# Performance work log

Hardware: AMD Instinct MI355X
Metric: run time of the kernel (lower is better)

## Reference

```python
import jax, jax.numpy as jnp
import numpy as np

D_MODEL = 2048
D_STATE = 64
D_CONV = 4
EXPAND = 2
HEADDIM = 64
NGROUPS = 1
CHUNK = 64
D_INNER = D_MODEL * EXPAND          # 4096
NHEADS = D_INNER // HEADDIM         # 64
D_IN_PROJ = 2 * D_INNER + 2 * NGROUPS * D_STATE + NHEADS
BATCH, SEQLEN = 2, 4096
RMS_EPS = 1e-6


def elu_plus_one(x):
    return jax.nn.elu(x) + 1.0


def softplus(x):
    return jnp.where(x > 20, x, jnp.log1p(jnp.exp(x)))


def causal_conv1d(x, w, b):
    # x: (B, L, D), w: (K, D) depthwise kernel, b: (D,)
    Bsz, L, Dn = x.shape
    k = w.shape[0]
    xp = jnp.transpose(jnp.pad(x, ((0, 0), (k - 1, 0), (0, 0))), (0, 2, 1))  # (B, D, L+K-1)
    kern = jnp.transpose(w, (1, 0))[:, None, :]  # (D, 1, K)
    y = jax.lax.conv_general_dilated(xp, kern, (1,), 'VALID',
                                     feature_group_count=Dn,
                                     dimension_numbers=('NCH', 'OIH', 'NCH'))
    return jnp.transpose(y, (0, 2, 1)) + b


def ssd_chunked(q, k, v, a, chunk_size):
    # SSD / chunked linear attention with per-step scalar decay.
    # Recurrence: h_t = a_t * h_{t-1} + k_t v_t^T ; y_t = q_t @ h_t
    # q,k: (B,H,L,N); v: (B,H,L,P); a: (B,H,L) in (0,1)
    Bsz, H, L, N = q.shape
    S = chunk_size
    C = L // S
    qc = q.reshape(Bsz, H, C, S, N)
    kc = k.reshape(Bsz, H, C, S, N)
    vc = v.reshape(Bsz, H, C, S, -1)
    la = jnp.log(a).reshape(Bsz, H, C, S)
    cs = jnp.cumsum(la, axis=-1)                 # inclusive cumsum of log-decay within chunk
    causal = jnp.tril(jnp.ones((S, S), bool))
    # decay from position j to i (j<=i): exp(cs_i - cs_j)
    logdec = jnp.where(causal, cs[..., :, None] - cs[..., None, :], -jnp.inf)
    att = jnp.einsum('bhcsn,bhctn->bhcst', qc, kc) * jnp.exp(logdec)
    y_intra = jnp.einsum('bhcst,bhctp->bhcsp', att, vc)
    total = cs[..., -1]                           # (B,H,C) total log-decay per chunk
    k_scaled = kc * jnp.exp(total[..., None, None] - cs[..., None])
    states = jnp.einsum('bhcsn,bhcsp->bhcnp', k_scaled, vc)  # per-chunk state update
    d_t = jnp.moveaxis(jnp.exp(total), 2, 0)      # (C,B,H)
    s_t = jnp.moveaxis(states, 2, 0)              # (C,B,H,N,P)

    def step(h, inp):
        d, s = inp
        return d[..., None, None] * h + s, h      # emit state at chunk start

    _, h_prev = jax.lax.scan(step, jnp.zeros_like(s_t[0]), (d_t, s_t))
    h_prev = jnp.moveaxis(h_prev, 0, 2)           # (B,H,C,N,P)
    y_inter = jnp.einsum('bhcsn,bhcnp->bhcsp', qc * jnp.exp(cs)[..., None], h_prev)
    return (y_intra + y_inter).reshape(Bsz, H, L, -1)


def setup_inputs() -> dict:
    key = jax.random.key(0)
    k0, k1, k2, k3 = jax.random.split(key, 4)
    u = jax.random.normal(k0, (BATCH, SEQLEN, D_MODEL), jnp.float32)
    in_proj_w = jax.random.normal(k1, (D_MODEL, D_IN_PROJ), jnp.float32) / np.sqrt(D_MODEL)
    conv_weight = jax.random.normal(k2, (D_CONV, D_INNER), jnp.float32) / np.sqrt(D_CONV)
    conv_bias = jnp.zeros((D_INNER,), jnp.float32)
    A_log = jnp.log(jnp.linspace(1.0, 16.0, NHEADS)).astype(jnp.float32)
    dt_init = jnp.exp(jnp.linspace(np.log(0.001), np.log(0.1), NHEADS))
    dt_bias = (dt_init + jnp.log(-jnp.expm1(-dt_init))).astype(jnp.float32)
    D_param = jnp.ones((NHEADS,), jnp.float32)
    norm_scale = jnp.ones((D_INNER,), jnp.float32)
    out_proj_w = jax.random.normal(k3, (D_INNER, D_MODEL), jnp.float32) / np.sqrt(D_INNER)
    return dict(u=u, in_proj_w=in_proj_w, conv_weight=conv_weight, conv_bias=conv_bias,
                A_log=A_log, dt_bias=dt_bias, D_param=D_param, norm_scale=norm_scale,
                out_proj_w=out_proj_w)


def reference(u, in_proj_w, conv_weight, conv_bias, A_log, dt_bias, D_param, norm_scale, out_proj_w):
    Bsz, L, _ = u.shape
    zxBCdt = u @ in_proj_w
    splits = [D_INNER, 2 * D_INNER, 2 * D_INNER + NGROUPS * D_STATE, 2 * D_INNER + 2 * NGROUPS * D_STATE]
    z, x, B_proj, C_proj, dt_logits = jnp.split(zxBCdt, splits, axis=-1)
    x = jax.nn.silu(causal_conv1d(x, conv_weight, conv_bias))
    B_mat = elu_plus_one(B_proj.reshape(Bsz, L, NGROUPS, D_STATE))
    C_mat = elu_plus_one(C_proj.reshape(Bsz, L, NGROUPS, D_STATE))
    hpg = NHEADS // NGROUPS
    B_mat = jnp.repeat(B_mat, hpg, axis=2)   # (B,L,H,N)
    C_mat = jnp.repeat(C_mat, hpg, axis=2)
    dt = softplus(dt_logits + dt_bias)        # (B,L,H)
    a = jnp.exp(-dt * jnp.exp(A_log))         # (B,L,H), per-step decay
    x_heads = x.reshape(Bsz, L, NHEADS, HEADDIM)
    q = jnp.transpose(C_mat, (0, 2, 1, 3))
    k = jnp.transpose(B_mat, (0, 2, 1, 3))
    v = jnp.transpose(x_heads, (0, 2, 1, 3))
    a_t = jnp.transpose(a, (0, 2, 1))
    y = ssd_chunked(q, k, v, a_t, CHUNK)
    y = y + D_param[None, :, None, None] * v  # skip connection
    y = jnp.transpose(y, (0, 2, 1, 3)).reshape(Bsz, L, D_INNER)
    y = y * jax.lax.rsqrt(jnp.mean(y * y, axis=-1, keepdims=True) + RMS_EPS) * norm_scale
    y = y * jax.nn.silu(z)
    return y @ out_proj_w
```

## Files before the change

### kernel.cpp

```cpp
#include <hip/hip_runtime.h>
#include <hip/hip_bf16.h>
#include <cstdint>
#include <cstddef>

#define BATCH   2
#define SEQLEN  4096
#define DMODEL  2048
#define DINNER  4096
#define NHEADS  64
#define HEADDIM 64
#define DSTATE  64
#define CHUNK   64
#define NCHUNK  (SEQLEN/CHUNK)
#define DPROJ   8384
#define DPROJ_PAD 8448
#define MTOK    (BATCH*SEQLEN)
#define RMS_EPS 1e-6f

typedef __hip_bfloat16 bf16;
typedef __attribute__((ext_vector_type(8))) short bf16x8;
typedef __attribute__((ext_vector_type(4))) float f32x4;

__device__ __forceinline__ float siluf(float x) { return x / (1.f + expf(-x)); }
__device__ __forceinline__ float to_f(float x) { return x; }
__device__ __forceinline__ float to_f(bf16 x) { return __bfloat162float(x); }
__device__ __forceinline__ float bf2f(short s) { bf16 h; *(short*)&h = s; return __bfloat162float(h); }
__device__ __forceinline__ void from_f(float& d, float x) { d = x; }
__device__ __forceinline__ void from_f(bf16& d, float x) { d = __float2bfloat16(x); }

__device__ __forceinline__ void gload16(const void* g, void* l) {
  __builtin_amdgcn_global_load_lds(
      (const __attribute__((address_space(1))) void*)g,
      (__attribute__((address_space(3))) void*)l, 16, 0, 0);
}

template <typename TC, int KT>
__global__ __launch_bounds__(1024, 4) void gemm_w16(
    const bf16* __restrict__ A, int lda,
    const bf16* __restrict__ BT, int ldb,
    TC* __restrict__ C, int ldc, int gx) {
  __shared__ __align__(16) bf16 As[4 * 8192];
  __shared__ __align__(16) bf16 Bs[4 * 8192];
  const int tid  = threadIdx.x;
  const int lane = tid & 63;
  const int w    = tid >> 6;
  const int wm   = w >> 2;
  const int wn   = w & 3;
  const int lr   = lane & 15, lg = lane >> 4;
  const int fo   = 8 * (lg ^ ((lr >> 1) & 3));

  int nwg = gridDim.x;
  int bid = (int)blockIdx.x;
  int idx = (bid & 7) * (nwg >> 3) + (bid >> 3);
  int spos = idx % (8 * gx);
  const int m0 = ((idx / (8 * gx)) * 8 + (spos & 7)) * 256;
  const int n0 = (spos >> 3) * 256;

  const int srow = tid >> 2;
  const int ce   = 8 * ((tid & 3) ^ ((tid >> 3) & 3));
  const bf16* pA = A  + (size_t)(m0 + srow) * lda + ce;
  const bf16* pB = BT + (size_t)(n0 + srow) * ldb + ce;
  const int wofs = w * 512;
  const int aRd = (wm * 64 + lr) * 32 + fo;
  const int bRd = (wn * 64 + lr) * 32 + fo;

#define STAGE_A(kt) gload16(pA + ((kt) << 5), As + (((kt) & 3) << 13) + wofs)
#define STAGE_B(kt) gload16(pB + ((kt) << 5), Bs + (((kt) & 3) << 13) + wofs)

  f32x4 acc[4][4];
#pragma unroll
  for (int m = 0; m < 4; ++m)
#pragma unroll
    for (int n = 0; n < 4; ++n) acc[m][n] = (f32x4){0.f, 0.f, 0.f, 0.f};

  bf16x8 fr[2][8];

#define RDFRAG(P, SL) do {                                                    \
    const bf16* Ab_ = As + ((SL) << 13);                                      \
    const bf16* Bb_ = Bs + ((SL) << 13);                                      \
    _Pragma("unroll")                                                         \
    for (int n = 0; n < 4; ++n) fr[P][4 + n] = *(const bf16x8*)&Bb_[bRd + n * 512]; \
    _Pragma("unroll")                                                         \
    for (int m = 0; m < 4; ++m) fr[P][m] = *(const bf16x8*)&Ab_[aRd + m * 512]; \
  } while (0)

#define KB(T, P, DOSTAGE, DOPF, VMC) do {                                     \
    if (DOSTAGE) { STAGE_A((T) + 3); STAGE_B((T) + 3); }                      \
    asm volatile("s_waitcnt lgkmcnt(0)" ::: "memory");                        \
    __builtin_amdgcn_sched_barrier(0);                                        \
    __builtin_amdgcn_s_setprio(1);                                            \
    _Pragma("unroll")                                                         \
    for (int m = 0; m < 4; ++m)                                               \
      _Pragma("unroll")                                                       \
      for (int n = 0; n < 4; ++n)                                             \
        acc[m][n] = __builtin_amdgcn_mfma_f32_16x16x32_bf16(fr[P][m], fr[P][4 + n], acc[m][n], 0, 0, 0); \
    __builtin_amdgcn_s_setprio(0);                                            \
    if (DOPF) {                                                               \
      asm volatile("s_waitcnt vmcnt(" #VMC ")" ::: "memory");                 \
      __builtin_amdgcn_sched_barrier(0);                                      \
      RDFRAG(1 - (P), ((T) + 1) & 3);                                         \
    }                                                                         \
    __builtin_amdgcn_s_barrier();                                             \
    __builtin_amdgcn_sched_barrier(0);                                        \
  } while (0)

  STAGE_A(0); STAGE_B(0); STAGE_A(1); STAGE_B(1); STAGE_A(2); STAGE_B(2);
  asm volatile("s_waitcnt vmcnt(4)" ::: "memory");
  __builtin_amdgcn_s_barrier();
  __builtin_amdgcn_sched_barrier(0);
  RDFRAG(0, 0);

  for (int t4 = 0; t4 < KT - 4; t4 += 4) {
    KB(t4 + 0, 0, true, true, 4);
    KB(t4 + 1, 1, true, true, 4);
    KB(t4 + 2, 0, true, true, 4);
    KB(t4 + 3, 1, true, true, 4);
  }
  KB(KT - 4, 0, true,  true,  4);
  KB(KT - 3, 1, false, true,  2);
  KB(KT - 2, 0, false, true,  0);
  KB(KT - 1, 1, false, false, 0);
#undef KB
#undef RDFRAG
#undef STAGE_A
#undef STAGE_B

  if constexpr (__is_same(TC, bf16)) {
    bf16* Ws = (w < 8 ? As : Bs) + (w & 7) * 4096;
#pragma unroll
    for (int m = 0; m < 4; ++m)
#pragma unroll
      for (int n = 0; n < 4; ++n)
#pragma unroll
        for (int reg = 0; reg < 4; ++reg) {
          int row = m * 16 + lg * 4 + reg;
          int slot = (n * 2 + (lr >> 3)) ^ (row & 7);
          Ws[row * 64 + slot * 8 + (lr & 7)] = __float2bfloat16(acc[m][n][reg]);
        }
    asm volatile("s_waitcnt lgkmcnt(0)" ::: "memory");
#pragma unroll
    for (int i = 0; i < 8; ++i) {
      int row = i * 8 + (lane >> 3);
      bf16x8 v = *(const bf16x8*)&Ws[row * 64 + ((lane & 7) ^ (lane >> 3)) * 8];
      int gcol = n0 + wn * 64 + (lane & 7) * 8;
      *(bf16x8*)&((bf16*)C)[(size_t)(m0 + wm * 64 + row) * ldc + gcol] = v;
    }
  } else {
#pragma unroll
    for (int m = 0; m < 4; ++m)
#pragma unroll
      for (int n = 0; n < 4; ++n) {
        int col = n0 + wn * 64 + n * 16 + lr;
        size_t rbase = (size_t)(m0 + wm * 64 + m * 16 + lg * 4);
#pragma unroll
        for (int reg = 0; reg < 4; ++reg)
          from_f(C[(rbase + reg) * ldc + col], acc[m][n][reg]);
      }
  }
}

template <typename TC, bool MASK>
__global__ __launch_bounds__(256) void gemm_mfma(
    const bf16* __restrict__ A, int lda,
    const bf16* __restrict__ BT, int ldb,
    TC* __restrict__ C, int ldc, int Kdim, int Nvalid) {
  __shared__ __align__(16) bf16 As[128 * 32];
  __shared__ __align__(16) bf16 Bs[128 * 32];
  const int tid  = threadIdx.x;
  const int lane = tid & 63;
  const int w    = tid >> 6;
  const int m0 = blockIdx.y * 128;
  const int n0 = blockIdx.x * 128;

  const int rs0 = w * 32 + (lane >> 2);
  const int ce  = 8 * ((lane & 3) ^ ((lane >> 2) & 3));
  const int fo  = 8 * ((lane >> 4) ^ (lane & 3));
  const int lr  = lane & 15, lg = lane >> 4;
  const int wr = w >> 1, wc = w & 1;

  f32x4 acc[4][4];
#pragma unroll
  for (int m = 0; m < 4; ++m)
#pragma unroll
    for (int n = 0; n < 4; ++n) acc[m][n] = (f32x4){0.f, 0.f, 0.f, 0.f};

  const size_t arow0 = (size_t)(m0 + rs0) * lda;
  const size_t arow1 = (size_t)(m0 + rs0 + 16) * lda;
  const size_t brow0 = (size_t)(n0 + rs0) * ldb;
  const size_t brow1 = (size_t)(n0 + rs0 + 16) * ldb;
  bf16* lA0 = &As[(w * 2 + 0) * 512];
  bf16* lA1 = &As[(w * 2 + 1) * 512];
  bf16* lB0 = &Bs[(w * 2 + 0) * 512];
  bf16* lB1 = &Bs[(w * 2 + 1) * 512];

  for (int k0 = 0; k0 < Kdim; k0 += 32) {
    __syncthreads();
    gload16(A + arow0 + k0 + ce, lA0);
    gload16(A + arow1 + k0 + ce, lA1);
    gload16(BT + brow0 + k0 + ce, lB0);
    gload16(BT + brow1 + k0 + ce, lB1);
    __syncthreads();
    bf16x8 af[4], bfr[4];
#pragma unroll
    for (int m = 0; m < 4; ++m)
      af[m] = *(const bf16x8*)&As[(wr * 64 + m * 16 + lr) * 32 + fo];
#pragma unroll
    for (int n = 0; n < 4; ++n)
      bfr[n] = *(const bf16x8*)&Bs[(wc * 64 + n * 16 + lr) * 32 + fo];
#pragma unroll
    for (int m = 0; m < 4; ++m)
#pragma unroll
      for (int n = 0; n < 4; ++n)
        acc[m][n] = __builtin_amdgcn_mfma_f32_16x16x32_bf16(af[m], bfr[n], acc[m][n], 0, 0, 0);
  }

#pragma unroll
  for (int m = 0; m < 4; ++m)
#pragma unroll
    for (int n = 0; n < 4; ++n) {
      int col = n0 + wc * 64 + n * 16 + lr;
      if (MASK && col >= Nvalid) continue;
      size_t rbase = (size_t)(m0 + wr * 64 + m * 16 + lg * 4);
#pragma unroll
      for (int reg = 0; reg < 4; ++reg)
        from_f(C[(rbase + reg) * ldc + col], acc[m][n][reg]);
    }
}

__global__ __launch_bounds__(256) void cast_bf16_kernel(
    const float* __restrict__ x, bf16* __restrict__ y) {
  size_t i = ((size_t)blockIdx.x * 256 + threadIdx.x) * 4;
  float4 v = *(const float4*)(x + i);
  y[i + 0] = __float2bfloat16(v.x);
  y[i + 1] = __float2bfloat16(v.y);
  y[i + 2] = __float2bfloat16(v.z);
  y[i + 3] = __float2bfloat16(v.w);
}

__global__ __launch_bounds__(256) void transpose_cast_kernel(
    const float* __restrict__ W, bf16* __restrict__ WT, int N, int K) {
  __shared__ float t[32][33];
  int n0 = blockIdx.x * 32, k0 = blockIdx.y * 32;
  int tx = threadIdx.x & 31, ty = threadIdx.x >> 5;
#pragma unroll
  for (int i = 0; i < 4; ++i) {
    int n = n0 + tx;
    t[ty + i * 8][tx] = (n < N) ? W[(size_t)(k0 + ty + i * 8) * N + n] : 0.f;
  }
  __syncthreads();
#pragma unroll
  for (int i = 0; i < 4; ++i) {
    int nn = ty + i * 8;
    WT[(size_t)(n0 + nn) * K + k0 + tx] = __float2bfloat16(t[tx][nn]);
  }
}

__global__ __launch_bounds__(256) void conv_silu_kernel(
    const bf16* __restrict__ zx, const float* __restrict__ cw,
    const float* __restrict__ cb, bf16* __restrict__ xc) {
  int idx = blockIdx.x * 256 + threadIdx.x;
  int d8 = (idx & 511) * 8;
  int g = idx >> 9;
  int m0 = g * 4;
  int l0 = m0 & (SEQLEN - 1);
  int b = m0 >> 12;
  bf16x8 rows[7];
  bf16x8 zvec;
#pragma unroll
  for (int j = 0; j < 8; ++j) zvec[j] = 0;
#pragma unroll
  for (int r = 0; r < 7; ++r) {
    int li = l0 - 3 + r;
    rows[r] = (li >= 0)
        ? *(const bf16x8*)&zx[(size_t)(b * SEQLEN + li) * DPROJ + DINNER + d8]
        : zvec;
  }
  float cwv[4][8], cbv[8];
#pragma unroll
  for (int k = 0; k < 4; ++k) {
    float4 a = *(const float4*)(cw + k * DINNER + d8);
    float4 bb = *(const float4*)(cw + k * DINNER + d8 + 4);
    cwv[k][0] = a.x; cwv[k][1] = a.y; cwv[k][2] = a.z; cwv[k][3] = a.w;
    cwv[k][4] = bb.x; cwv[k][5] = bb.y; cwv[k][6] = bb.z; cwv[k][7] = bb.w;
  }
  {
    float4 a = *(const float4*)(cb + d8);
    float4 bb = *(const float4*)(cb + d8 + 4);
    cbv[0] = a.x; cbv[1] = a.y; cbv[2] = a.z; cbv[3] = a.w;
    cbv[4] = bb.x; cbv[5] = bb.y; cbv[6] = bb.z; cbv[7] = bb.w;
  }
#pragma unroll
  for (int j = 0; j < 4; ++j) {
    float acc[8];
#pragma unroll
    for (int e = 0; e < 8; ++e) acc[e] = cbv[e];
#pragma unroll
    for (int k = 0; k < 4; ++k)
#pragma unroll
      for (int e = 0; e < 8; ++e) acc[e] += bf2f(rows[j + k][e]) * cwv[k][e];
    bf16x8 o;
#pragma unroll
    for (int e = 0; e < 8; ++e) { bf16 h = __float2bfloat16(siluf(acc[e])); o[e] = *(short*)&h; }
    *(bf16x8*)&xc[(size_t)(m0 + j) * DINNER + d8] = o;
  }
}

__global__ __launch_bounds__(256) void prep_cumsum_kernel(
    const bf16* __restrict__ zx, const float* __restrict__ A_log,
    const float* __restrict__ dt_bias, bf16* __restrict__ Bmb,
    bf16* __restrict__ Cmb, float* __restrict__ cs) {
  int bid = blockIdx.x;
  int c = bid & 63, b = bid >> 6;
  int m0 = b * SEQLEN + c * CHUNK;
  int tid = threadIdx.x;
  int s = tid >> 2, grp = (tid & 3) * 16;
  __shared__ float laT[64 * 65];
  __shared__ float segs[4][64];
  const bf16* row = zx + (size_t)(m0 + s) * DPROJ + 2 * DINNER;
  {
    union { bf16x8 v[2]; bf16 hh[16]; } u, o;
    u.v[0] = *(const bf16x8*)&row[grp];
    u.v[1] = *(const bf16x8*)&row[grp + 8];
#pragma unroll
    for (int i = 0; i < 16; ++i) {
      float bv = to_f(u.hh[i]);
      from_f(o.hh[i], bv > 0.f ? bv + 1.f : expf(bv));
    }
    *(bf16x8*)&Bmb[(size_t)(m0 + s) * 64 + grp] = o.v[0];
    *(bf16x8*)&Bmb[(size_t)(m0 + s) * 64 + grp + 8] = o.v[1];
    u.v[0] = *(const bf16x8*)&row[64 + grp];
    u.v[1] = *(const bf16x8*)&row[64 + grp + 8];
#pragma unroll
    for (int i = 0; i < 16; ++i) {
      float cv = to_f(u.hh[i]);
      from_f(o.hh[i], cv > 0.f ? cv + 1.f : expf(cv));
    }
    *(bf16x8*)&Cmb[(size_t)(m0 + s) * 64 + grp] = o.v[0];
    *(bf16x8*)&Cmb[(size_t)(m0 + s) * 64 + grp + 8] = o.v[1];
    u.v[0] = *(const bf16x8*)&row[128 + grp];
    u.v[1] = *(const bf16x8*)&row[128 + grp + 8];
#pragma unroll
    for (int i = 0; i < 16; ++i) {
      int j = grp + i;
      float dtl = to_f(u.hh[i]) + dt_bias[j];
      float dt = dtl > 20.f ? dtl : log1pf(expf(dtl));
      laT[j * 65 + s] = -dt * expf(A_log[j]);
    }
  }
  __syncthreads();
  int j = tid & 63, sg = tid >> 6;
  float p = 0.f;
#pragma unroll
  for (int i = 0; i < 16; ++i) p += laT[j * 65 + sg * 16 + i];
  segs[sg][j] = p;
  __syncthreads();
  float off = (sg > 0 ? segs[0][j] : 0.f) + (sg > 1 ? segs[1][j] : 0.f) +
              (sg > 2 ? segs[2][j] : 0.f);
  float acc = off;
#pragma unroll
  for (int i = 0; i < 16; ++i) {
    acc += laT[j * 65 + sg * 16 + i];
    cs[(size_t)(m0 + sg * 16 + i) * 64 + j] = acc;
  }
}

__global__ __launch_bounds__(256) void states_mfma(
    const bf16* __restrict__ Bmb, const bf16* __restrict__ xc,
    const float* __restrict__ cs, bf16* __restrict__ st) {
  int bid = blockIdx.x;
  int c = bid & 63, h = (bid >> 6) & 63, b = bid >> 12;
  int m0 = b * SEQLEN + c * CHUNK;
  int tid = threadIdx.x, lane = tid & 63, w = tid >> 6;
  int lr = lane & 15, lg = lane >> 4;
  __shared__ bf16 vT[64 * 72];
  __shared__ bf16 kT[64 * 72];
  int s4 = tid >> 2, c16 = (tid & 3) * 16;
  float cstot = cs[(size_t)(m0 + 63) * 64 + h];
  float ws = expf(cstot - cs[(size_t)(m0 + s4) * 64 + h]);
  {
    union { bf16x8 v[2]; bf16 hh[16]; } u;
    const bf16x8* pv = (const bf16x8*)&xc[(size_t)(m0 + s4) * DINNER + h * 64 + c16];
    u.v[0] = pv[0]; u.v[1] = pv[1];
#pragma unroll
    for (int i = 0; i < 16; ++i) vT[(c16 + i) * 72 + s4] = u.hh[i];
    const bf16x8* pk = (const bf16x8*)&Bmb[(size_t)(m0 + s4) * 64 + c16];
    u.v[0] = pk[0]; u.v[1] = pk[1];
#pragma unroll
    for (int i = 0; i < 16; ++i) kT[(c16 + i) * 72 + s4] = __float2bfloat16(to_f(u.hh[i]) * ws);
  }
  __syncthreads();
  f32x4 acc[4];
#pragma unroll
  for (int ct = 0; ct < 4; ++ct) acc[ct] = (f32x4){0.f, 0.f, 0.f, 0.f};
#pragma unroll
  for (int ks = 0; ks < 2; ++ks) {
    bf16x8 af = *(const bf16x8*)&vT[(w * 16 + lr) * 72 + ks * 32 + lg * 8];
#pragma unroll
    for (int ct = 0; ct < 4; ++ct) {
      bf16x8 bf_ = *(const bf16x8*)&kT[(ct * 16 + lr) * 72 + ks * 32 + lg * 8];
      acc[ct] = __builtin_amdgcn_mfma_f32_16x16x32_bf16(af, bf_, acc[ct], 0, 0, 0);
    }
  }
  size_t ob = (((size_t)(b * NHEADS + h)) * NCHUNK + c) * 4096;
#pragma unroll
  for (int ct = 0; ct < 4; ++ct) {
    int n = ct * 16 + lr;
#pragma unroll
    for (int r = 0; r < 4; ++r) {
      int p = w * 16 + lg * 4 + r;
      from_f(st[ob + (size_t)p * 64 + n], acc[ct][r]);
    }
  }
}

__global__ __launch_bounds__(256) void scan_kernel(
    const float* __restrict__ cs, bf16* __restrict__ st) {
  int bid = blockIdx.x;
  int bh = bid >> 2, qq = bid & 3;
  int b = bh >> 6, h = bh & 63;
  int tid = threadIdx.x;
  __shared__ float dec[64];
  if (tid < 64)
    dec[tid] = expf(cs[(size_t)(b * SEQLEN + tid * CHUNK + 63) * 64 + h]);
  int e0 = qq * 1024 + tid * 4;
  float hr[4] = {0.f, 0.f, 0.f, 0.f};
  size_t base = (size_t)bh * NCHUNK * 4096;
  typedef __attribute__((ext_vector_type(4))) short bf16x4;
  union U { bf16x4 v; bf16 hh[4]; };
  U buf[4];
  buf[0].v = *(bf16x4*)(st + base + 0 * 4096 + e0);
  buf[1].v = *(bf16x4*)(st + base + 1 * 4096 + e0);
  buf[2].v = *(bf16x4*)(st + base + 2 * 4096 + e0);
  __syncthreads();
#pragma unroll 4
  for (int c = 0; c < NCHUNK; ++c) {
    if (c + 3 < NCHUNK)
      buf[(c + 3) & 3].v = *(bf16x4*)(st + base + (size_t)(c + 3) * 4096 + e0);
    float d = dec[c];
    U out;
#pragma unroll
    for (int i = 0; i < 4; ++i) {
      float sv = to_f(buf[c & 3].hh[i]);
      from_f(out.hh[i], hr[i]);
      hr[i] = d * hr[i] + sv;
    }
    *(bf16x4*)(st + base + (size_t)c * 4096 + e0) = out.v;
  }
}

__global__ __launch_bounds__(256) void chunk_out_mfma(
    const bf16* __restrict__ Bmb, const bf16* __restrict__ Cmb,
    const bf16* __restrict__ xc, const float* __restrict__ cs,
    const bf16* __restrict__ st, const float* __restrict__ Dp,
    bf16* __restrict__ zx) {
  int bid = blockIdx.x;
  int c = bid & 63, h = (bid >> 6) & 63, b = bid >> 12;
  int m0 = b * SEQLEN + c * CHUNK;
  int tid = threadIdx.x, lane = tid & 63, w = tid >> 6;
  int lr = lane & 15, lg = lane >> 4;
  __shared__ bf16 qL[64 * 72];
  __shared__ bf16 kL[64 * 72];
  __shared__ bf16 A2[64 * 136];
  __shared__ bf16 B2[64 * 136];
  __shared__ float csl[64];
  int s4 = tid >> 2, c16 = (tid & 3) * 16;

  if (tid < 64) csl[tid] = cs[(size_t)(m0 + tid) * 64 + h];
  {
    const bf16x8* pq = (const bf16x8*)&Cmb[(size_t)(m0 + s4) * 64 + c16];
    *(bf16x8*)&qL[s4 * 72 + c16] = pq[0];
    *(bf16x8*)&qL[s4 * 72 + c16 + 8] = pq[1];
    const bf16x8* pk = (const bf16x8*)&Bmb[(size_t)(m0 + s4) * 64 + c16];
    *(bf16x8*)&kL[s4 * 72 + c16] = pk[0];
    *(bf16x8*)&kL[s4 * 72 + c16 + 8] = pk[1];
  }
  {
    union { bf16x8 v[2]; bf16 hh[16]; } u;
    const bf16x8* pv = (const bf16x8*)&xc[(size_t)(m0 + s4) * DINNER + h * 64 + c16];
    u.v[0] = pv[0]; u.v[1] = pv[1];
#pragma unroll
    for (int i = 0; i < 16; ++i) B2[(c16 + i) * 136 + s4] = u.hh[i];
  }
  {
    size_t hb = (((size_t)(b * NHEADS + h)) * NCHUNK + c) * 4096;
    const bf16x8* ph = (const bf16x8*)&st[hb + (size_t)s4 * 64 + c16];
    *(bf16x8*)&B2[s4 * 136 + 64 + c16] = ph[0];
    *(bf16x8*)&B2[s4 * 136 + 64 + c16 + 8] = ph[1];
  }
  __syncthreads();

  f32x4 acc1[4];
#pragma unroll
  for (int ct = 0; ct < 4; ++ct) acc1[ct] = (f32x4){0.f, 0.f, 0.f, 0.f};
#pragma unroll
  for (int ks = 0; ks < 2; ++ks) {
    bf16x8 af = *(const bf16x8*)&qL[(w * 16 + lr) * 72 + ks * 32 + lg * 8];
#pragma unroll
    for (int ct = 0; ct < 4; ++ct) {
      bf16x8 bf_ = *(const bf16x8*)&kL[(ct * 16 + lr) * 72 + ks * 32 + lg * 8];
      acc1[ct] = __builtin_amdgcn_mfma_f32_16x16x32_bf16(af, bf_, acc1[ct], 0, 0, 0);
    }
  }
  {
    float es = expf(csl[s4]);
    union { bf16x8 v[2]; bf16 hh[16]; } u;
    const bf16x8* pq = (const bf16x8*)&qL[s4 * 72 + c16];
    u.v[0] = pq[0]; u.v[1] = pq[1];
#pragma unroll
    for (int i = 0; i < 16; ++i) u.hh[i] = __float2bfloat16(to_f(u.hh[i]) * es);
    *(bf16x8*)&A2[s4 * 136 + 64 + c16] = u.v[0];
    *(bf16x8*)&A2[s4 * 136 + 64 + c16 + 8] = u.v[1];
  }
#pragma unroll
  for (int ct = 0; ct < 4; ++ct) {
    int t = ct * 16 + lr;
#pragma unroll
    for (int r = 0; r < 4; ++r) {
      int s = w * 16 + lg * 4 + r;
      float val = (t <= s) ? acc1[ct][r] * expf(csl[s] - csl[t]) : 0.f;
      A2[s * 136 + t] = __float2bfloat16(val);
    }
  }
  __syncthreads();

  float Dh = Dp[h];
  f32x4 acc2[4];
#pragma unroll
  for (int ct = 0; ct < 4; ++ct) {
    int p = ct * 16 + lr;
#pragma unroll
    for (int r = 0; r < 4; ++r)
      acc2[ct][r] = Dh * to_f(B2[p * 136 + (w * 16 + lg * 4 + r)]);
  }
#pragma unroll
  for (int ks = 0; ks < 4; ++ks) {
    bf16x8 af = *(const bf16x8*)&A2[(w * 16 + lr) * 136 + ks * 32 + lg * 8];
#pragma unroll
    for (int ct = 0; ct < 4; ++ct) {
      bf16x8 bf_ = *(const bf16x8*)&B2[(ct * 16 + lr) * 136 + ks * 32 + lg * 8];
      acc2[ct] = __builtin_amdgcn_mfma_f32_16x16x32_bf16(af, bf_, acc2[ct], 0, 0, 0);
    }
  }
  __syncthreads();
#pragma unroll
  for (int ct = 0; ct < 4; ++ct) {
    int p = ct * 16 + lr;
#pragma unroll
    for (int r = 0; r < 4; ++r)
      qL[(w * 16 + lg * 4 + r) * 72 + p] = __float2bfloat16(acc2[ct][r]);
  }
  __syncthreads();
  {
    const bf16x8* py = (const bf16x8*)&qL[s4 * 72 + c16];
    bf16x8* pg = (bf16x8*)&zx[(size_t)(m0 + s4) * DPROJ + DINNER + h * 64 + c16];
    pg[0] = py[0]; pg[1] = py[1];
  }
}

__global__ __launch_bounds__(256) void rmsnorm_gate_kernel(
    bf16* __restrict__ zx, const float* __restrict__ scale) {
  int m = blockIdx.x;
  int tid = threadIdx.x;
  bf16* row = zx + (size_t)m * DPROJ;
  float vals[16];
  float ss = 0.f;
#pragma unroll
  for (int g = 0; g < 2; ++g) {
    int d8 = (tid + g * 256) * 8;
    bf16x8 yv = *(const bf16x8*)&row[DINNER + d8];
#pragma unroll
    for (int j = 0; j < 8; ++j) {
      float y = bf2f(yv[j]);
      vals[g * 8 + j] = y;
      ss += y * y;
    }
  }
#pragma unroll
  for (int off = 32; off > 0; off >>= 1) ss += __shfl_down(ss, off, 64);
  __shared__ float red[4];
  if ((tid & 63) == 0) red[tid >> 6] = ss;
  __syncthreads();
  float tot = red[0] + red[1] + red[2] + red[3];
  float inv = rsqrtf(tot / (float)DINNER + RMS_EPS);
#pragma unroll
  for (int g = 0; g < 2; ++g) {
    int d8 = (tid + g * 256) * 8;
    bf16x8 zv = *(const bf16x8*)&row[d8];
    const float* sc = scale + d8;
    bf16x8 o;
#pragma unroll
    for (int j = 0; j < 8; ++j) {
      bf16 hh = __float2bfloat16(vals[g * 8 + j] * inv * sc[j] * siluf(bf2f(zv[j])));
      o[j] = *(short*)&hh;
    }
    *(bf16x8*)&row[DINNER + d8] = o;
  }
}

extern "C" void kernel_launch(void* const* d_in, const int* in_sizes, int n_in,
                              void* d_out, int out_size, void* d_ws, size_t ws_size,
                              hipStream_t stream) {
  const float* u       = (const float*)d_in[0];
  const float* Win     = (const float*)d_in[1];
  const float* cw      = (const float*)d_in[2];
  const float* cb      = (const float*)d_in[3];
  const float* A_log   = (const float*)d_in[4];
  const float* dt_bias = (const float*)d_in[5];
  const float* Dp      = (const float*)d_in[6];
  const float* nscale  = (const float*)d_in[7];
  const float* Wout    = (const float*)d_in[8];
  float* out = (float*)d_out;

  bf16* zx = (bf16*)d_ws;
  bf16* xc = zx + (size_t)MTOK * DPROJ;
  bf16* ub = xc;
  bf16* wT = xc + (size_t)MTOK * DINNER;
  bf16* Bmb = wT + (size_t)DPROJ_PAD * DMODEL;
  bf16* Cmb = Bmb + (size_t)MTOK * 64;
  float* cs = (float*)(Cmb + (size_t)MTOK * 64);
  bf16* st = (bf16*)d_out;

  cast_bf16_kernel<<<(MTOK * DMODEL) / (256 * 4), 256, 0, stream>>>(u, ub);
  transpose_cast_kernel<<<dim3(DPROJ_PAD / 32, DMODEL / 32), 256, 0, stream>>>(Win, wT, DPROJ, DMODEL);
  gemm_w16<bf16, DMODEL / 32><<<(2 * DINNER / 256) * (MTOK / 256), 1024, 0, stream>>>(
      ub, DMODEL, wT, DMODEL, zx, DPROJ, 2 * DINNER / 256);
  gemm_mfma<bf16, true><<<dim3(2, MTOK / 128), 256, 0, stream>>>(
      ub, DMODEL, wT + (size_t)(2 * DINNER) * DMODEL, DMODEL,
      zx + 2 * DINNER, DPROJ, DMODEL, 192);
  transpose_cast_kernel<<<dim3(DMODEL / 32, DINNER / 32), 256, 0, stream>>>(Wout, wT, DMODEL, DINNER);
  conv_silu_kernel<<<(MTOK / 4) * 512 / 256, 256, 0, stream>>>(zx, cw, cb, xc);
  prep_cumsum_kernel<<<BATCH * NCHUNK, 256, 0, stream>>>(zx, A_log, dt_bias, Bmb, Cmb, cs);
  states_mfma<<<BATCH * NHEADS * NCHUNK, 256, 0, stream>>>(Bmb, xc, cs, st);
  scan_kernel<<<BATCH * NHEADS * 4, 256, 0, stream>>>(cs, st);
  chunk_out_mfma<<<BATCH * NHEADS * NCHUNK, 256, 0, stream>>>(Bmb, Cmb, xc, cs, st, Dp, zx);
  rmsnorm_gate_kernel<<<MTOK, 256, 0, stream>>>(zx, nscale);
  gemm_w16<float, DINNER / 32><<<(DMODEL / 256) * (MTOK / 256), 1024, 0, stream>>>(
      zx + DINNER, DPROJ, wT, DINNER, out, DMODEL, DMODEL / 256);
}
```

Baseline: 650.1 us.

## Fuse chunk-state, scan and chunk-output into one sequential SSD kernel

Replaces the separate per-chunk state kernel, inter-chunk scan kernel and chunk output kernel with one fused kernel. Each block owns one (batch, head, half of headdim) slice and walks all chunks in order, keeping the running state in registers and shared memory. This removes the global round-trip of per-chunk states and two launches, but leaves only 256 blocks, each running a long serial loop with barriers and unprefetched global loads per chunk. The GEMM main loop also drops its double-buffered register fragment prefetch in favor of loading fragments from LDS each step, which may expose LDS latency before the MFMAs.

```diff
diff --git a/kernel.cpp b/kernel.cpp
--- a/kernel.cpp
+++ b/kernel.cpp
@@ -73,55 +73,40 @@
 #pragma unroll
     for (int n = 0; n < 4; ++n) acc[m][n] = (f32x4){0.f, 0.f, 0.f, 0.f};
 
-  bf16x8 fr[2][8];
-
-#define RDFRAG(P, SL) do {                                                    \
-    const bf16* Ab_ = As + ((SL) << 13);                                      \
-    const bf16* Bb_ = Bs + ((SL) << 13);                                      \
-    _Pragma("unroll")                                                         \
-    for (int n = 0; n < 4; ++n) fr[P][4 + n] = *(const bf16x8*)&Bb_[bRd + n * 512]; \
-    _Pragma("unroll")                                                         \
-    for (int m = 0; m < 4; ++m) fr[P][m] = *(const bf16x8*)&Ab_[aRd + m * 512]; \
-  } while (0)
-
-#define KB(T, P, DOSTAGE, DOPF, VMC) do {                                     \
-    if (DOSTAGE) { STAGE_A((T) + 3); STAGE_B((T) + 3); }                      \
-    asm volatile("s_waitcnt lgkmcnt(0)" ::: "memory");                        \
-    __builtin_amdgcn_sched_barrier(0);                                        \
-    __builtin_amdgcn_s_setprio(1);                                            \
-    _Pragma("unroll")                                                         \
-    for (int m = 0; m < 4; ++m)                                               \
-      _Pragma("unroll")                                                       \
-      for (int n = 0; n < 4; ++n)                                             \
-        acc[m][n] = __builtin_amdgcn_mfma_f32_16x16x32_bf16(fr[P][m], fr[P][4 + n], acc[m][n], 0, 0, 0); \
-    __builtin_amdgcn_s_setprio(0);                                            \
-    if (DOPF) {                                                               \
-      asm volatile("s_waitcnt vmcnt(" #VMC ")" ::: "memory");                 \
-      __builtin_amdgcn_sched_barrier(0);                                      \
-      RDFRAG(1 - (P), ((T) + 1) & 3);                                         \
-    }                                                                         \
-    __builtin_amdgcn_s_barrier();                                             \
-    __builtin_amdgcn_sched_barrier(0);                                        \
+#define KBODY(T, DOSTAGE, VMC) do {                                          \
+    const bf16* Ab = As + (((T) & 3) << 13);                                 \
+    const bf16* Bb = Bs + (((T) & 3) << 13);                                 \
+    if (DOSTAGE) { STAGE_A((T) + 3); STAGE_B((T) + 3); }                     \
+    bf16x8 bfv[4], af[4];                                                    \
+    _Pragma("unroll")                                                        \
+    for (int n = 0; n < 4; ++n) bfv[n] = *(const bf16x8*)&Bb[bRd + n * 512]; \
+    _Pragma("unroll")                                                        \
+    for (int m = 0; m < 4; ++m) af[m] = *(const bf16x8*)&Ab[aRd + m * 512];  \
+    asm volatile("s_waitcnt lgkmcnt(0)" ::: "memory");                       \
+    __builtin_amdgcn_sched_barrier(0);                                       \
+    __builtin_amdgcn_s_setprio(1);                                           \
+    _Pragma("unroll")                                                        \
+    for (int m = 0; m < 4; ++m)                                              \
+      _Pragma("unroll")                                                      \
+      for (int n = 0; n < 4; ++n)                                            \
+        acc[m][n] = __builtin_amdgcn_mfma_f32_16x16x32_bf16(af[m], bfv[n], acc[m][n], 0, 0, 0); \
+    __builtin_amdgcn_s_setprio(0);                                           \
+    asm volatile("s_waitcnt vmcnt(" #VMC ")" ::: "memory");                  \
+    __builtin_amdgcn_s_barrier();                                            \
+    __builtin_amdgcn_sched_barrier(0);                                       \
   } while (0)
 
   STAGE_A(0); STAGE_B(0); STAGE_A(1); STAGE_B(1); STAGE_A(2); STAGE_B(2);
   asm volatile("s_waitcnt vmcnt(4)" ::: "memory");
   __builtin_amdgcn_s_barrier();
   __builtin_amdgcn_sched_barrier(0);
-  RDFRAG(0, 0);
-
-  for (int t4 = 0; t4 < KT - 4; t4 += 4) {
-    KB(t4 + 0, 0, true, true, 4);
-    KB(t4 + 1, 1, true, true, 4);
-    KB(t4 + 2, 0, true, true, 4);
-    KB(t4 + 3, 1, true, true, 4);
-  }
-  KB(KT - 4, 0, true,  true,  4);
-  KB(KT - 3, 1, false, true,  2);
-  KB(KT - 2, 0, false, true,  0);
-  KB(KT - 1, 1, false, false, 0);
-#undef KB
-#undef RDFRAG
+
+#pragma unroll 4
+  for (int t = 0; t < KT - 3; ++t) KBODY(t, true, 4);
+  KBODY(KT - 3, false, 2);
+  KBODY(KT - 2, false, 0);
+  KBODY(KT - 1, false, 0);
+#undef KBODY
 #undef STAGE_A
 #undef STAGE_B
 
@@ -364,196 +349,138 @@
   }
 }
 
-__global__ __launch_bounds__(256) void states_mfma(
-    const bf16* __restrict__ Bmb, const bf16* __restrict__ xc,
-    const float* __restrict__ cs, bf16* __restrict__ st) {
+__global__ __launch_bounds__(256, 2) void ssd_fused(
+    const bf16* __restrict__ Bmb, const bf16* __restrict__ Cmb,
+    const bf16* __restrict__ xc, const float* __restrict__ cs,
+    const float* __restrict__ Dp, bf16* __restrict__ zx) {
   int bid = blockIdx.x;
-  int c = bid & 63, h = (bid >> 6) & 63, b = bid >> 12;
-  int m0 = b * SEQLEN + c * CHUNK;
+  int ph = bid & 1, h = (bid >> 1) & 63, b = bid >> 7;
   int tid = threadIdx.x, lane = tid & 63, w = tid >> 6;
   int lr = lane & 15, lg = lane >> 4;
-  __shared__ bf16 vT[64 * 72];
-  __shared__ bf16 kT[64 * 72];
-  int s4 = tid >> 2, c16 = (tid & 3) * 16;
-  float cstot = cs[(size_t)(m0 + 63) * 64 + h];
-  float ws = expf(cstot - cs[(size_t)(m0 + s4) * 64 + h]);
-  {
-    union { bf16x8 v[2]; bf16 hh[16]; } u;
-    const bf16x8* pv = (const bf16x8*)&xc[(size_t)(m0 + s4) * DINNER + h * 64 + c16];
-    u.v[0] = pv[0]; u.v[1] = pv[1];
-#pragma unroll
-    for (int i = 0; i < 16; ++i) vT[(c16 + i) * 72 + s4] = u.hh[i];
-    const bf16x8* pk = (const bf16x8*)&Bmb[(size_t)(m0 + s4) * 64 + c16];
-    u.v[0] = pk[0]; u.v[1] = pk[1];
-#pragma unroll
-    for (int i = 0; i < 16; ++i) kT[(c16 + i) * 72 + s4] = __float2bfloat16(to_f(u.hh[i]) * ws);
-  }
-  __syncthreads();
-  f32x4 acc[4];
-#pragma unroll
-  for (int ct = 0; ct < 4; ++ct) acc[ct] = (f32x4){0.f, 0.f, 0.f, 0.f};
-#pragma unroll
-  for (int ks = 0; ks < 2; ++ks) {
-    bf16x8 af = *(const bf16x8*)&vT[(w * 16 + lr) * 72 + ks * 32 + lg * 8];
-#pragma unroll
-    for (int ct = 0; ct < 4; ++ct) {
-      bf16x8 bf_ = *(const bf16x8*)&kT[(ct * 16 + lr) * 72 + ks * 32 + lg * 8];
-      acc[ct] = __builtin_amdgcn_mfma_f32_16x16x32_bf16(af, bf_, acc[ct], 0, 0, 0);
-    }
-  }
-  size_t ob = (((size_t)(b * NHEADS + h)) * NCHUNK + c) * 4096;
-#pragma unroll
-  for (int ct = 0; ct < 4; ++ct) {
-    int n = ct * 16 + lr;
-#pragma unroll
-    for (int r = 0; r < 4; ++r) {
-      int p = w * 16 + lg * 4 + r;
-      from_f(st[ob + (size_t)p * 64 + n], acc[ct][r]);
-    }
-  }
-}
-
-__global__ __launch_bounds__(256) void scan_kernel(
-    const float* __restrict__ cs, bf16* __restrict__ st) {
-  int bid = blockIdx.x;
-  int bh = bid >> 2, qq = bid & 3;
-  int b = bh >> 6, h = bh & 63;
-  int tid = threadIdx.x;
-  __shared__ float dec[64];
-  if (tid < 64)
-    dec[tid] = expf(cs[(size_t)(b * SEQLEN + tid * CHUNK + 63) * 64 + h]);
-  int e0 = qq * 1024 + tid * 4;
-  float hr[4] = {0.f, 0.f, 0.f, 0.f};
-  size_t base = (size_t)bh * NCHUNK * 4096;
-  typedef __attribute__((ext_vector_type(4))) short bf16x4;
-  union U { bf16x4 v; bf16 hh[4]; };
-  U buf[4];
-  buf[0].v = *(bf16x4*)(st + base + 0 * 4096 + e0);
-  buf[1].v = *(bf16x4*)(st + base + 1 * 4096 + e0);
-  buf[2].v = *(bf16x4*)(st + base + 2 * 4096 + e0);
-  __syncthreads();
-#pragma unroll 4
-  for (int c = 0; c < NCHUNK; ++c) {
-    if (c + 3 < NCHUNK)
-      buf[(c + 3) & 3].v = *(bf16x4*)(st + base + (size_t)(c + 3) * 4096 + e0);
-    float d = dec[c];
-    U out;
-#pragma unroll
-    for (int i = 0; i < 4; ++i) {
-      float sv = to_f(buf[c & 3].hh[i]);
-      from_f(out.hh[i], hr[i]);
-      hr[i] = d * hr[i] + sv;
-    }
-    *(bf16x4*)(st + base + (size_t)c * 4096 + e0) = out.v;
-  }
-}
-
-__global__ __launch_bounds__(256) void chunk_out_mfma(
-    const bf16* __restrict__ Bmb, const bf16* __restrict__ Cmb,
-    const bf16* __restrict__ xc, const float* __restrict__ cs,
-    const bf16* __restrict__ st, const float* __restrict__ Dp,
-    bf16* __restrict__ zx) {
-  int bid = blockIdx.x;
-  int c = bid & 63, h = (bid >> 6) & 63, b = bid >> 12;
-  int m0 = b * SEQLEN + c * CHUNK;
-  int tid = threadIdx.x, lane = tid & 63, w = tid >> 6;
-  int lr = lane & 15, lg = lane >> 4;
+  int pt = w & 1, nh = w >> 1;
   __shared__ bf16 qL[64 * 72];
   __shared__ bf16 kL[64 * 72];
+  __shared__ bf16 kscL[64 * 72];
+  __shared__ bf16 B2[32 * 136];
   __shared__ bf16 A2[64 * 136];
-  __shared__ bf16 B2[64 * 136];
   __shared__ float csl[64];
-  int s4 = tid >> 2, c16 = (tid & 3) * 16;
-
-  if (tid < 64) csl[tid] = cs[(size_t)(m0 + tid) * 64 + h];
+  int s4 = tid >> 2, c16 = (tid & 3) * 16, pg = (tid & 3) * 8;
+  float Dh = Dp[h];
+
   {
-    const bf16x8* pq = (const bf16x8*)&Cmb[(size_t)(m0 + s4) * 64 + c16];
-    *(bf16x8*)&qL[s4 * 72 + c16] = pq[0];
-    *(bf16x8*)&qL[s4 * 72 + c16 + 8] = pq[1];
-    const bf16x8* pk = (const bf16x8*)&Bmb[(size_t)(m0 + s4) * 64 + c16];
-    *(bf16x8*)&kL[s4 * 72 + c16] = pk[0];
-    *(bf16x8*)&kL[s4 * 72 + c16 + 8] = pk[1];
-  }
-  {
-    union { bf16x8 v[2]; bf16 hh[16]; } u;
-    const bf16x8* pv = (const bf16x8*)&xc[(size_t)(m0 + s4) * DINNER + h * 64 + c16];
-    u.v[0] = pv[0]; u.v[1] = pv[1];
-#pragma unroll
-    for (int i = 0; i < 16; ++i) B2[(c16 + i) * 136 + s4] = u.hh[i];
-  }
-  {
-    size_t hb = (((size_t)(b * NHEADS + h)) * NCHUNK + c) * 4096;
-    const bf16x8* ph = (const bf16x8*)&st[hb + (size_t)s4 * 64 + c16];
-    *(bf16x8*)&B2[s4 * 136 + 64 + c16] = ph[0];
-    *(bf16x8*)&B2[s4 * 136 + 64 + c16 + 8] = ph[1];
-  }
-  __syncthreads();
-
-  f32x4 acc1[4];
-#pragma unroll
-  for (int ct = 0; ct < 4; ++ct) acc1[ct] = (f32x4){0.f, 0.f, 0.f, 0.f};
-#pragma unroll
-  for (int ks = 0; ks < 2; ++ks) {
-    bf16x8 af = *(const bf16x8*)&qL[(w * 16 + lr) * 72 + ks * 32 + lg * 8];
+    int pr = tid >> 3, c8 = (tid & 7) * 8;
+    bf16x8 z;
+#pragma unroll
+    for (int j = 0; j < 8; ++j) z[j] = 0;
+    *(bf16x8*)&B2[pr * 136 + 64 + c8] = z;
+  }
+  f32x4 acc_h[2];
+  acc_h[0] = (f32x4){0.f, 0.f, 0.f, 0.f};
+  acc_h[1] = (f32x4){0.f, 0.f, 0.f, 0.f};
+
+  for (int c = 0; c < NCHUNK; ++c) {
+    int m0 = b * SEQLEN + c * CHUNK;
+    if (tid < 64) csl[tid] = cs[(size_t)(m0 + tid) * 64 + h];
+    {
+      const bf16x8* pq = (const bf16x8*)&Cmb[(size_t)(m0 + s4) * 64 + c16];
+      *(bf16x8*)&qL[s4 * 72 + c16] = pq[0];
+      *(bf16x8*)&qL[s4 * 72 + c16 + 8] = pq[1];
+      union { bf16x8 v[2]; bf16 hh[16]; } u;
+      const bf16x8* pk = (const bf16x8*)&Bmb[(size_t)(m0 + s4) * 64 + c16];
+      u.v[0] = pk[0]; u.v[1] = pk[1];
+      *(bf16x8*)&kL[s4 * 72 + c16] = u.v[0];
+      *(bf16x8*)&kL[s4 * 72 + c16 + 8] = u.v[1];
+      float cstot = cs[(size_t)(m0 + 63) * 64 + h];
+      float ws = expf(cstot - cs[(size_t)(m0 + s4) * 64 + h]);
+#pragma unroll
+      for (int i = 0; i < 16; ++i)
+        kscL[(c16 + i) * 72 + s4] = __float2bfloat16(to_f(u.hh[i]) * ws);
+      union { bf16x8 v; bf16 hh[8]; } uv;
+      uv.v = *(const bf16x8*)&xc[(size_t)(m0 + s4) * DINNER + h * 64 + ph * 32 + pg];
+#pragma unroll
+      for (int i = 0; i < 8; ++i) B2[(pg + i) * 136 + s4] = uv.hh[i];
+    }
+    __syncthreads();
+    f32x4 acc1[4];
+#pragma unroll
+    for (int ct = 0; ct < 4; ++ct) acc1[ct] = (f32x4){0.f, 0.f, 0.f, 0.f};
+#pragma unroll
+    for (int ks = 0; ks < 2; ++ks) {
+      bf16x8 af = *(const bf16x8*)&qL[(w * 16 + lr) * 72 + ks * 32 + lg * 8];
+#pragma unroll
+      for (int ct = 0; ct < 4; ++ct) {
+        bf16x8 bf_ = *(const bf16x8*)&kL[(ct * 16 + lr) * 72 + ks * 32 + lg * 8];
+        acc1[ct] = __builtin_amdgcn_mfma_f32_16x16x32_bf16(af, bf_, acc1[ct], 0, 0, 0);
+      }
+    }
+    {
+      float es = expf(csl[s4]);
+      union { bf16x8 v[2]; bf16 hh[16]; } u;
+      const bf16x8* pq = (const bf16x8*)&qL[s4 * 72 + c16];
+      u.v[0] = pq[0]; u.v[1] = pq[1];
+#pragma unroll
+      for (int i = 0; i < 16; ++i) u.hh[i] = __float2bfloat16(to_f(u.hh[i]) * es);
+      *(bf16x8*)&A2[s4 * 136 + 64 + c16] = u.v[0];
+      *(bf16x8*)&A2[s4 * 136 + 64 + c16 + 8] = u.v[1];
+    }
 #pragma unroll
     for (int ct = 0; ct < 4; ++ct) {
-      bf16x8 bf_ = *(const bf16x8*)&kL[(ct * 16 + lr) * 72 + ks * 32 + lg * 8];
-      acc1[ct] = __builtin_amdgcn_mfma_f32_16x16x32_bf16(af, bf_, acc1[ct], 0, 0, 0);
-    }
-  }
-  {
-    float es = expf(csl[s4]);
-    union { bf16x8 v[2]; bf16 hh[16]; } u;
-    const bf16x8* pq = (const bf16x8*)&qL[s4 * 72 + c16];
-    u.v[0] = pq[0]; u.v[1] = pq[1];
-#pragma unroll
-    for (int i = 0; i < 16; ++i) u.hh[i] = __float2bfloat16(to_f(u.hh[i]) * es);
-    *(bf16x8*)&A2[s4 * 136 + 64 + c16] = u.v[0];
-    *(bf16x8*)&A2[s4 * 136 + 64 + c16 + 8] = u.v[1];
-  }
-#pragma unroll
-  for (int ct = 0; ct < 4; ++ct) {
-    int t = ct * 16 + lr;
-#pragma unroll
-    for (int r = 0; r < 4; ++r) {
-      int s = w * 16 + lg * 4 + r;
-      float val = (t <= s) ? acc1[ct][r] * expf(csl[s] - csl[t]) : 0.f;
-      A2[s * 136 + t] = __float2bfloat16(val);
-    }
-  }
-  __syncthreads();
-
-  float Dh = Dp[h];
-  f32x4 acc2[4];
-#pragma unroll
-  for (int ct = 0; ct < 4; ++ct) {
-    int p = ct * 16 + lr;
-#pragma unroll
-    for (int r = 0; r < 4; ++r)
-      acc2[ct][r] = Dh * to_f(B2[p * 136 + (w * 16 + lg * 4 + r)]);
-  }
-#pragma unroll
-  for (int ks = 0; ks < 4; ++ks) {
-    bf16x8 af = *(const bf16x8*)&A2[(w * 16 + lr) * 136 + ks * 32 + lg * 8];
-#pragma unroll
-    for (int ct = 0; ct < 4; ++ct) {
-      bf16x8 bf_ = *(const bf16x8*)&B2[(ct * 16 + lr) * 136 + ks * 32 + lg * 8];
-      acc2[ct] = __builtin_amdgcn_mfma_f32_16x16x32_bf16(af, bf_, acc2[ct], 0, 0, 0);
-    }
-  }
-  __syncthreads();
-#pragma unroll
-  for (int ct = 0; ct < 4; ++ct) {
-    int p = ct * 16 + lr;
-#pragma unroll
-    for (int r = 0; r < 4; ++r)
-      qL[(w * 16 + lg * 4 + r) * 72 + p] = __float2bfloat16(acc2[ct][r]);
-  }
-  __syncthreads();
-  {
-    const bf16x8* py = (const bf16x8*)&qL[s4 * 72 + c16];
-    bf16x8* pg = (bf16x8*)&zx[(size_t)(m0 + s4) * DPROJ + DINNER + h * 64 + c16];
-    pg[0] = py[0]; pg[1] = py[1];
+      int t = ct * 16 + lr;
+#pragma unroll
+      for (int r = 0; r < 4; ++r) {
+        int s = w * 16 + lg * 4 + r;
+        float val = (t <= s) ? acc1[ct][r] * expf(csl[s] - csl[t]) : 0.f;
+        A2[s * 136 + t] = __float2bfloat16(val);
+      }
+    }
+    __syncthreads();
+    f32x4 acc2[2];
+#pragma unroll
+    for (int ct = 0; ct < 2; ++ct) {
+      int p = ct * 16 + lr;
+#pragma unroll
+      for (int r = 0; r < 4; ++r)
+        acc2[ct][r] = Dh * to_f(B2[p * 136 + (w * 16 + lg * 4 + r)]);
+    }
+#pragma unroll
+    for (int ks = 0; ks < 4; ++ks) {
+      bf16x8 af = *(const bf16x8*)&A2[(w * 16 + lr) * 136 + ks * 32 + lg * 8];
+#pragma unroll
+      for (int ct = 0; ct < 2; ++ct) {
+        bf16x8 bf_ = *(const bf16x8*)&B2[(ct * 16 + lr) * 136 + ks * 32 + lg * 8];
+        acc2[ct] = __builtin_amdgcn_mfma_f32_16x16x32_bf16(af, bf_, acc2[ct], 0, 0, 0);
+      }
+    }
+    {
+      float dtot = expf(csl[63]);
+#pragma unroll
+      for (int ct = 0; ct < 2; ++ct)
+#pragma unroll
+        for (int r = 0; r < 4; ++r) acc_h[ct][r] *= dtot;
+#pragma unroll
+      for (int ks = 0; ks < 2; ++ks) {
+        bf16x8 af = *(const bf16x8*)&B2[(pt * 16 + lr) * 136 + ks * 32 + lg * 8];
+#pragma unroll
+        for (int ct = 0; ct < 2; ++ct) {
+          bf16x8 bf_ = *(const bf16x8*)&kscL[(nh * 32 + ct * 16 + lr) * 72 + ks * 32 + lg * 8];
+          acc_h[ct] = __builtin_amdgcn_mfma_f32_16x16x32_bf16(af, bf_, acc_h[ct], 0, 0, 0);
+        }
+      }
+    }
+    __syncthreads();
+#pragma unroll
+    for (int ct = 0; ct < 2; ++ct)
+#pragma unroll
+      for (int r = 0; r < 4; ++r) {
+        B2[(pt * 16 + lg * 4 + r) * 136 + 64 + nh * 32 + ct * 16 + lr] =
+            __float2bfloat16(acc_h[ct][r]);
+        A2[(w * 16 + lg * 4 + r) * 136 + ct * 16 + lr] = __float2bfloat16(acc2[ct][r]);
+      }
+    __syncthreads();
+    {
+      bf16x8 yv = *(const bf16x8*)&A2[s4 * 136 + pg];
+      *(bf16x8*)&zx[(size_t)(m0 + s4) * DPROJ + DINNER + h * 64 + ph * 32 + pg] = yv;
+    }
   }
 }
 
@@ -618,7 +545,6 @@
   bf16* Bmb = wT + (size_t)DPROJ_PAD * DMODEL;
   bf16* Cmb = Bmb + (size_t)MTOK * 64;
   float* cs = (float*)(Cmb + (size_t)MTOK * 64);
-  bf16* st = (bf16*)d_out;
 
   cast_bf16_kernel<<<(MTOK * DMODEL) / (256 * 4), 256, 0, stream>>>(u, ub);
   transpose_cast_kernel<<<dim3(DPROJ_PAD / 32, DMODEL / 32), 256, 0, stream>>>(Win, wT, DPROJ, DMODEL);
@@ -630,9 +556,7 @@
   transpose_cast_kernel<<<dim3(DMODEL / 32, DINNER / 32), 256, 0, stream>>>(Wout, wT, DMODEL, DINNER);
   conv_silu_kernel<<<(MTOK / 4) * 512 / 256, 256, 0, stream>>>(zx, cw, cb, xc);
   prep_cumsum_kernel<<<BATCH * NCHUNK, 256, 0, stream>>>(zx, A_log, dt_bias, Bmb, Cmb, cs);
-  states_mfma<<<BATCH * NHEADS * NCHUNK, 256, 0, stream>>>(Bmb, xc, cs, st);
-  scan_kernel<<<BATCH * NHEADS * 4, 256, 0, stream>>>(cs, st);
-  chunk_out_mfma<<<BATCH * NHEADS * NCHUNK, 256, 0, stream>>>(Bmb, Cmb, xc, cs, st, Dp, zx);
+  ssd_fused<<<BATCH * NHEADS * 2, 256, 0, stream>>>(Bmb, Cmb, xc, cs, Dp, zx);
   rmsnorm_gate_kernel<<<MTOK, 256, 0, stream>>>(zx, nscale);
   gemm_w16<float, DINNER / 32><<<(DMODEL / 256) * (MTOK / 256), 1024, 0, stream>>>(
       zx + DINNER, DPROJ, wT, DINNER, out, DMODEL, DMODEL / 256);
```

After: 738.3 us. +13.6%, slower.
